# Kernel optimization log

Measured on AMD Instinct MI355X. Metric: run time of the kernel, lower is better.

The kernel has to match this reference:

```python
import jax, jax.numpy as jnp
import numpy as np

HID = 256
N_LAYERS = 4
DT = 0.05
EPS = 1e-3
TMAX = 50


def setup_inputs() -> dict:
    key = jax.random.key(0)
    ks = jax.random.split(key, 7)
    B, S, D = 8, 1024, HID
    s1 = 1.0 / np.sqrt(D)      # fan_in = D for w_state / w_input
    s2 = 1.0 / np.sqrt(2 * D)  # fan_in = 2D for tau_gate linear
    x = jax.random.normal(ks[0], (B, S, D), dtype=jnp.float32)
    Ws = jax.random.uniform(ks[1], (N_LAYERS, D, D), jnp.float32, -s1, s1)
    bs = jax.random.uniform(ks[2], (N_LAYERS, D), jnp.float32, -s1, s1)
    Wi = jax.random.uniform(ks[3], (N_LAYERS, D, D), jnp.float32, -s1, s1)
    bi = jax.random.uniform(ks[4], (N_LAYERS, D), jnp.float32, -s1, s1)
    Wt = jax.random.uniform(ks[5], (N_LAYERS, D, 2 * D), jnp.float32, -s2, s2)
    bt = jax.random.uniform(ks[6], (N_LAYERS, D), jnp.float32, -s2, s2)
    return {"x": x, "Ws": Ws, "bs": bs, "Wi": Wi, "bi": bi, "Wt": Wt, "bt": bt}


def _run(x, Ws, bs, Wi, bi, Wt, bt):
    B, S, D = x.shape

    def layer_fn(cur_in, layer):
        h_prev, Ws_i, bs_i, Wi_i, bi_i, Wt_i, bt_i = layer
        combined = jnp.concatenate([cur_in, h_prev], axis=-1)          # [B,S,2D]
        tau = jax.nn.sigmoid(jnp.einsum('bsk,dk->bsd', combined, Wt_i) + bt_i)
        forcing = jnp.tanh(
            jnp.einsum('bsd,ed->bse', h_prev, Ws_i) + bs_i
            + jnp.einsum('bsd,ed->bse', cur_in, Wi_i) + bi_i
        )
        h_new = jnp.clip(h_prev + DT * (-h_prev / (tau + 1e-6) + forcing), -10.0, 10.0)
        delta = jnp.max(jnp.abs(h_new - h_prev))
        return h_new, (h_new, delta)

    @jax.checkpoint
    def step(carry, i):
        states, result, done = carry
        _, (new_states, deltas) = jax.lax.scan(
            layer_fn, x, (states, Ws, bs, Wi, bi, Wt, bt))
        converged = jnp.max(deltas) < EPS
        states = jnp.where(done, states, new_states)
        # torch returns loop index t at the first converging iteration, else TMAX
        result = jnp.where(done | ~converged, result, i)
        done = done | converged
        return (states, result, done), None

    init = (jnp.zeros((N_LAYERS, B, S, D), x.dtype),
            jnp.array(TMAX, jnp.int32),
            jnp.array(False))
    (states, result, _), _ = jax.lax.scan(step, init, jnp.arange(TMAX, dtype=jnp.int32))
    return states[-1], result


def reference(x, Ws, bs, Wi, bi, Wt, bt):
    return _run(x, Ws, bs, Wi, bi, Wt, bt)
```

## Files before the change

kernel.cpp:

```cpp
#include <hip/hip_runtime.h>
#include <math.h>

#define HID 256
#define TWOH 512
#define ROWS 8192
#define NLAYER 4
#define TMAX 50
#define DT 0.05f
#define EPSC 1e-3f

typedef float f32x4 __attribute__((ext_vector_type(4)));
typedef unsigned char u8;

__device__ inline u8 f32_to_fp8(float v) {
    return (u8)(__builtin_amdgcn_cvt_pk_fp8_f32(v, v, 0, 0) & 0xff);
}
__device__ inline float fp8_to_f32(u8 b) {
    return __builtin_amdgcn_cvt_f32_fp8((int)b, 0);
}

__global__ void pack_w_kernel(const float* __restrict__ Ws,
                              const float* __restrict__ Wi,
                              const float* __restrict__ Wt,
                              u8* __restrict__ Wf) {
    int e = blockIdx.x * 256 + threadIdx.x;
    int j    = e & 7;
    int lane = (e >> 3) & 63;
    int nt   = (e >> 9) & 3;
    int ci   = (e >> 11) & 15;
    int wv   = (e >> 15) & 7;
    int L    = (e >> 18);
    int l15  = lane & 15;
    int quad = lane >> 4;
    int d = wv * 32 + (nt & 1) * 16 + l15;
    int k = ci * 32 + quad * 8 + j;
    float v;
    if ((nt >> 1) == 0) {
        v = Wt[(size_t)L * HID * TWOH + (size_t)d * TWOH + k];
    } else {
        v = (k < HID) ? Wi[(size_t)L * HID * HID + (size_t)d * HID + k]
                      : Ws[(size_t)L * HID * HID + (size_t)d * HID + (k - HID)];
    }
    Wf[e] = f32_to_fp8(v);
}

__global__ void pack_b_kernel(const float* __restrict__ bs,
                              const float* __restrict__ bi,
                              const float* __restrict__ bt,
                              float* __restrict__ bp) {
    int idx = blockIdx.x * 256 + threadIdx.x;
    int L = idx / TWOH;
    int n = idx % TWOH;
    int d = n >> 1;
    bp[idx] = ((n & 1) == 0) ? bt[L * HID + d]
                             : (bs[L * HID + d] + bi[L * HID + d]);
}

__global__ __launch_bounds__(512, 1) void persistent_kernel(
    const float* __restrict__ x,
    const u8* __restrict__ Wf,
    const float* __restrict__ bp,
    float* __restrict__ deltas,
    float* __restrict__ out)
{
    __shared__ u8 sX[32 * 256];
    __shared__ u8 sH[NLAYER][32 * 256];
    __shared__ float2 sBias[NLAYER][256];
    __shared__ float sRed[8];

    const int tid  = threadIdx.x;
    const int lane = tid & 63;
    const int wv   = tid >> 6;
    const int l15  = lane & 15;
    const int quad = lane >> 4;
    const int w32  = wv * 32;
    const size_t rowbase = (size_t)blockIdx.x * 32;

    #pragma unroll
    for (int it = 0; it < 2; ++it) {
        int s = tid + it * 512;
        int r = s >> 5, seg = s & 31;
        const float* gx = x + (rowbase + r) * HID + seg * 8;
        float4 v0 = *(const float4*)gx;
        float4 v1 = *(const float4*)(gx + 4);
        int lo = __builtin_amdgcn_cvt_pk_fp8_f32(v0.x, v0.y, 0, 0);
        lo     = __builtin_amdgcn_cvt_pk_fp8_f32(v0.z, v0.w, lo, 1);
        int hi = __builtin_amdgcn_cvt_pk_fp8_f32(v1.x, v1.y, 0, 0);
        hi     = __builtin_amdgcn_cvt_pk_fp8_f32(v1.z, v1.w, hi, 1);
        long pk = ((long)(unsigned int)lo) | ((long)hi << 32);
        *(long*)&sX[r * 256 + (seg ^ r) * 8] = pk;
    }
    {
        long* hflat = (long*)&sH[0][0];
        #pragma unroll
        for (int it = 0; it < 8; ++it) hflat[tid + it * 512] = 0;
    }
    #pragma unroll
    for (int it = 0; it < 2; ++it) {
        int i = tid + it * 512;
        sBias[i >> 8][i & 255] = *(const float2*)(bp + (i >> 8) * TWOH + 2 * (i & 255));
    }

    __syncthreads();

    for (int t = 0; t < TMAX; ++t) {
        float dmax = 0.0f;
        for (int L = 0; L < NLAYER; ++L) {
            const u8* Alo = (L == 0) ? sX : sH[L - 1];
            u8*       Ahi = sH[L];
            const u8* wb = Wf + ((size_t)(L * 8 + wv) * 32768) + (size_t)lane * 8;

            f32x4 acc[2][4];
            #pragma unroll
            for (int mt = 0; mt < 2; ++mt)
                #pragma unroll
                for (int nt = 0; nt < 4; ++nt)
                    acc[mt][nt] = (f32x4){0.f, 0.f, 0.f, 0.f};

            long bb[4][4];
            #pragma unroll
            for (int pi = 0; pi < 4; ++pi)
                #pragma unroll
                for (int nt = 0; nt < 4; ++nt)
                    bb[pi][nt] = *(const long*)(wb + (size_t)(pi * 4 + nt) * 512);

            #pragma unroll
            for (int ci = 0; ci < 16; ++ci) {
                const int p = ci & 3;
                const u8* Asrc = (ci < 8) ? Alo : Ahi;
                const int seg = (ci & 7) * 4 + quad;
                long a[2];
                #pragma unroll
                for (int mt = 0; mt < 2; ++mt) {
                    int row = mt * 16 + l15;
                    a[mt] = *(const long*)&Asrc[row * 256 + (seg ^ row) * 8];
                }
                #pragma unroll
                for (int mt = 0; mt < 2; ++mt)
                    #pragma unroll
                    for (int nt = 0; nt < 4; ++nt)
                        acc[mt][nt] = __builtin_amdgcn_mfma_f32_16x16x32_fp8_fp8(
                            a[mt], bb[p][nt], acc[mt][nt], 0, 0, 0);
                if (ci + 4 < 16) {
                    #pragma unroll
                    for (int nt = 0; nt < 4; ++nt)
                        bb[p][nt] = *(const long*)(wb + (size_t)((ci + 4) * 4 + nt) * 512);
                }
            }

            __syncthreads();

            #pragma unroll
            for (int ntp = 0; ntp < 2; ++ntp) {
                const int d = w32 + ntp * 16 + l15;
                const float2 bb2 = sBias[L][d];
                const int seg = d >> 3, dlow = d & 7;
                #pragma unroll
                for (int mt = 0; mt < 2; ++mt) {
                    #pragma unroll
                    for (int r = 0; r < 4; ++r) {
                        float tpre = acc[mt][ntp][r]     + bb2.x;
                        float fpre = acc[mt][ntp + 2][r] + bb2.y;
                        tpre = fminf(30.f, fmaxf(-30.f, tpre));
                        fpre = fminf(15.f, fmaxf(-15.f, fpre));
                        float u   = __expf(-tpre);
                        float den = 1.0f + 1e-6f + 1e-6f * u;
                        float rcp = __builtin_amdgcn_rcpf(den);
                        float e2  = __expf(2.0f * fpre);
                        float r2  = __builtin_amdgcn_rcpf(e2 + 1.0f);
                        float fo  = (e2 - 1.0f) * r2;
                        const int row = mt * 16 + quad * 4 + r;
                        const int idx = row * 256 + (seg ^ row) * 8 + dlow;
                        float h  = fp8_to_f32(Ahi[idx]);
                        float g  = h * (1.0f + u) * rcp;
                        float nv = h + DT * (fo - g);
                        nv = fminf(10.0f, fmaxf(-10.0f, nv));
                        Ahi[idx] = f32_to_fp8(nv);
                        dmax = fmaxf(dmax, fabsf(nv - h));
                    }
                }
            }
            if (L == NLAYER - 1) {
                #pragma unroll
                for (int off = 32; off > 0; off >>= 1)
                    dmax = fmaxf(dmax, __shfl_xor(dmax, off));
                if (lane == 0) sRed[wv] = dmax;
            }
            __syncthreads();
        }

        if (tid == 0) {
            float m = sRed[0];
            #pragma unroll
            for (int w = 1; w < 8; ++w) m = fmaxf(m, sRed[w]);
            atomicMax((unsigned int*)(deltas + t), __float_as_uint(m));
        }
    }

    #pragma unroll
    for (int it = 0; it < 2; ++it) {
        int s = tid + it * 512;
        int r = s >> 5, seg = s & 31;
        long v = *(const long*)&sH[NLAYER - 1][r * 256 + (seg ^ r) * 8];
        int lo = (int)(v & 0xffffffffl);
        int hi = (int)(v >> 32);
        float* go = out + (rowbase + r) * HID + seg * 8;
        float4 o0, o1;
        o0.x = __builtin_amdgcn_cvt_f32_fp8(lo, 0);
        o0.y = __builtin_amdgcn_cvt_f32_fp8(lo, 1);
        o0.z = __builtin_amdgcn_cvt_f32_fp8(lo, 2);
        o0.w = __builtin_amdgcn_cvt_f32_fp8(lo, 3);
        o1.x = __builtin_amdgcn_cvt_f32_fp8(hi, 0);
        o1.y = __builtin_amdgcn_cvt_f32_fp8(hi, 1);
        o1.z = __builtin_amdgcn_cvt_f32_fp8(hi, 2);
        o1.w = __builtin_amdgcn_cvt_f32_fp8(hi, 3);
        *(float4*)go = o0;
        *(float4*)(go + 4) = o1;
    }
}

__global__ void result_kernel(const float* __restrict__ deltas,
                              float* __restrict__ out) {
    if (threadIdx.x == 0) {
        int res = TMAX;
        for (int t = 0; t < TMAX; ++t) {
            if (deltas[t] < EPSC) { res = t; break; }
        }
        out[(size_t)ROWS * HID] = (float)res;
    }
}

extern "C" void kernel_launch(void* const* d_in, const int* in_sizes, int n_in,
                              void* d_out, int out_size, void* d_ws, size_t ws_size,
                              hipStream_t stream) {
    const float* x  = (const float*)d_in[0];
    const float* Ws = (const float*)d_in[1];
    const float* bs = (const float*)d_in[2];
    const float* Wi = (const float*)d_in[3];
    const float* bi = (const float*)d_in[4];
    const float* Wt = (const float*)d_in[5];
    const float* bt = (const float*)d_in[6];
    float* out = (float*)d_out;

    char* p = (char*)d_ws;
    u8*    Wf     = (u8*)p;    p += (size_t)NLAYER * TWOH * TWOH;
    float* bp     = (float*)p; p += (size_t)NLAYER * TWOH * sizeof(float);
    float* deltas = (float*)p; p += 64 * sizeof(float);

    hipMemsetAsync(deltas, 0, 64 * sizeof(float), stream);
    pack_w_kernel<<<(NLAYER * TWOH * TWOH) / 256, 256, 0, stream>>>(Ws, Wi, Wt, Wf);
    pack_b_kernel<<<(NLAYER * TWOH) / 256, 256, 0, stream>>>(bs, bi, bt, bp);

    persistent_kernel<<<256, 512, 0, stream>>>(x, Wf, bp, deltas, out);
    result_kernel<<<1, 64, 0, stream>>>(deltas, out);
}
```

Measured before the change: 1.228 ms.

## Double-buffer hidden states to cut per-layer barriers and widen weight loads

Hidden states are now ping-pong buffered across timesteps. Each layer reads the previous timestep's own-layer state first and syncs only once, midway, before reading the lower layer's new state. This removes one of the two block barriers per layer. The weight packing is reordered so each lane loads 16-byte vectors instead of 8-byte ones. The per-wave delta max now goes straight to a global atomic instead of through a shared reduction, which adds more atomics per block and doubles the hidden-state shared memory.

```diff
diff --git a/kernel.cpp b/kernel.cpp
--- a/kernel.cpp
+++ b/kernel.cpp
@@ -10,6 +10,7 @@
 #define EPSC 1e-3f
 
 typedef float f32x4 __attribute__((ext_vector_type(4)));
+typedef long  long2v __attribute__((ext_vector_type(2)));
 typedef unsigned char u8;
 
 __device__ inline u8 f32_to_fp8(float v) {
@@ -25,17 +26,18 @@
                               u8* __restrict__ Wf) {
     int e = blockIdx.x * 256 + threadIdx.x;
     int j    = e & 7;
-    int lane = (e >> 3) & 63;
-    int nt   = (e >> 9) & 3;
+    int h    = (e >> 3) & 1;
+    int lane = (e >> 4) & 63;
+    int g    = (e >> 10) & 1;
     int ci   = (e >> 11) & 15;
     int wv   = (e >> 15) & 7;
     int L    = (e >> 18);
     int l15  = lane & 15;
     int quad = lane >> 4;
-    int d = wv * 32 + (nt & 1) * 16 + l15;
+    int d = wv * 32 + h * 16 + l15;
     int k = ci * 32 + quad * 8 + j;
     float v;
-    if ((nt >> 1) == 0) {
+    if (g == 0) {
         v = Wt[(size_t)L * HID * TWOH + (size_t)d * TWOH + k];
     } else {
         v = (k < HID) ? Wi[(size_t)L * HID * HID + (size_t)d * HID + k]
@@ -64,9 +66,8 @@
     float* __restrict__ out)
 {
     __shared__ u8 sX[32 * 256];
-    __shared__ u8 sH[NLAYER][32 * 256];
+    __shared__ u8 sH[2][NLAYER][32 * 256];
     __shared__ float2 sBias[NLAYER][256];
-    __shared__ float sRed[8];
 
     const int tid  = threadIdx.x;
     const int lane = tid & 63;
@@ -91,9 +92,9 @@
         *(long*)&sX[r * 256 + (seg ^ r) * 8] = pk;
     }
     {
-        long* hflat = (long*)&sH[0][0];
+        long* hflat = (long*)&sH[0][0][0];
         #pragma unroll
-        for (int it = 0; it < 8; ++it) hflat[tid + it * 512] = 0;
+        for (int it = 0; it < 16; ++it) hflat[tid + it * 512] = 0;
     }
     #pragma unroll
     for (int it = 0; it < 2; ++it) {
@@ -103,64 +104,69 @@
 
     __syncthreads();
 
+    #pragma unroll 1
     for (int t = 0; t < TMAX; ++t) {
+        const int rs = t & 1, ws = rs ^ 1;
         float dmax = 0.0f;
+        #pragma unroll
         for (int L = 0; L < NLAYER; ++L) {
-            const u8* Alo = (L == 0) ? sX : sH[L - 1];
-            u8*       Ahi = sH[L];
-            const u8* wb = Wf + ((size_t)(L * 8 + wv) * 32768) + (size_t)lane * 8;
+            const u8* Ahi = &sH[rs][L][0];
+            const u8* Alo = (L == 0) ? sX : &sH[ws][L - 1][0];
+            u8*       Hout = &sH[ws][L][0];
+            const u8* wb = Wf + ((size_t)(L * 8 + wv) << 15) + (size_t)lane * 16;
 
             f32x4 acc[2][4];
             #pragma unroll
             for (int mt = 0; mt < 2; ++mt)
                 #pragma unroll
-                for (int nt = 0; nt < 4; ++nt)
-                    acc[mt][nt] = (f32x4){0.f, 0.f, 0.f, 0.f};
-
-            long bb[4][4];
-            #pragma unroll
-            for (int pi = 0; pi < 4; ++pi)
-                #pragma unroll
-                for (int nt = 0; nt < 4; ++nt)
-                    bb[pi][nt] = *(const long*)(wb + (size_t)(pi * 4 + nt) * 512);
-
-            #pragma unroll
-            for (int ci = 0; ci < 16; ++ci) {
-                const int p = ci & 3;
-                const u8* Asrc = (ci < 8) ? Alo : Ahi;
+                for (int n = 0; n < 4; ++n)
+                    acc[mt][n] = (f32x4){0.f, 0.f, 0.f, 0.f};
+
+            long2v bb[2][2];
+            #pragma unroll
+            for (int pi = 0; pi < 2; ++pi)
+                #pragma unroll
+                for (int g = 0; g < 2; ++g)
+                    bb[pi][g] = *(const long2v*)(wb + (size_t)(((8 + pi) * 2 + g) << 10));
+
+            #pragma unroll
+            for (int s = 0; s < 16; ++s) {
+                const int ci = (s < 8) ? (s + 8) : (s - 8);
+                const int p = s & 1;
+                if (s == 8) __syncthreads();
+                const u8* Asrc = (s < 8) ? Ahi : Alo;
                 const int seg = (ci & 7) * 4 + quad;
                 long a[2];
                 #pragma unroll
                 for (int mt = 0; mt < 2; ++mt) {
-                    int row = mt * 16 + l15;
+                    const int row = mt * 16 + l15;
                     a[mt] = *(const long*)&Asrc[row * 256 + (seg ^ row) * 8];
                 }
                 #pragma unroll
                 for (int mt = 0; mt < 2; ++mt)
                     #pragma unroll
-                    for (int nt = 0; nt < 4; ++nt)
-                        acc[mt][nt] = __builtin_amdgcn_mfma_f32_16x16x32_fp8_fp8(
-                            a[mt], bb[p][nt], acc[mt][nt], 0, 0, 0);
-                if (ci + 4 < 16) {
+                    for (int n = 0; n < 4; ++n)
+                        acc[mt][n] = __builtin_amdgcn_mfma_f32_16x16x32_fp8_fp8(
+                            a[mt], bb[p][n >> 1][n & 1], acc[mt][n], 0, 0, 0);
+                if (s + 2 < 16) {
+                    const int nci = (s + 2 < 8) ? (s + 10) : (s - 6);
                     #pragma unroll
-                    for (int nt = 0; nt < 4; ++nt)
-                        bb[p][nt] = *(const long*)(wb + (size_t)((ci + 4) * 4 + nt) * 512);
+                    for (int g = 0; g < 2; ++g)
+                        bb[p][g] = *(const long2v*)(wb + (size_t)((nci * 2 + g) << 10));
                 }
             }
 
-            __syncthreads();
-
             #pragma unroll
             for (int ntp = 0; ntp < 2; ++ntp) {
                 const int d = w32 + ntp * 16 + l15;
-                const float2 bb2 = sBias[L][d];
+                const float2 b2 = sBias[L][d];
                 const int seg = d >> 3, dlow = d & 7;
                 #pragma unroll
                 for (int mt = 0; mt < 2; ++mt) {
                     #pragma unroll
                     for (int r = 0; r < 4; ++r) {
-                        float tpre = acc[mt][ntp][r]     + bb2.x;
-                        float fpre = acc[mt][ntp + 2][r] + bb2.y;
+                        float tpre = acc[mt][ntp][r]     + b2.x;
+                        float fpre = acc[mt][ntp + 2][r] + b2.y;
                         tpre = fminf(30.f, fmaxf(-30.f, tpre));
                         fpre = fminf(15.f, fmaxf(-15.f, fpre));
                         float u   = __expf(-tpre);
@@ -172,10 +178,10 @@
                         const int row = mt * 16 + quad * 4 + r;
                         const int idx = row * 256 + (seg ^ row) * 8 + dlow;
                         float h  = fp8_to_f32(Ahi[idx]);
-                        float g  = h * (1.0f + u) * rcp;
-                        float nv = h + DT * (fo - g);
+                        float gq = h * (1.0f + u) * rcp;
+                        float nv = h + DT * (fo - gq);
                         nv = fminf(10.0f, fmaxf(-10.0f, nv));
-                        Ahi[idx] = f32_to_fp8(nv);
+                        Hout[idx] = f32_to_fp8(nv);
                         dmax = fmaxf(dmax, fabsf(nv - h));
                     }
                 }
@@ -184,38 +190,36 @@
                 #pragma unroll
                 for (int off = 32; off > 0; off >>= 1)
                     dmax = fmaxf(dmax, __shfl_xor(dmax, off));
-                if (lane == 0) sRed[wv] = dmax;
+                if (lane == 0)
+                    atomicMax((unsigned int*)(deltas + t), __float_as_uint(dmax));
             }
-            __syncthreads();
         }
-
-        if (tid == 0) {
-            float m = sRed[0];
-            #pragma unroll
-            for (int w = 1; w < 8; ++w) m = fmaxf(m, sRed[w]);
-            atomicMax((unsigned int*)(deltas + t), __float_as_uint(m));
+    }
+
+    __syncthreads();
+
+    {
+        const u8* fin = &sH[((TMAX - 1) & 1) ^ 1][NLAYER - 1][0];
+        #pragma unroll
+        for (int it = 0; it < 2; ++it) {
+            int s = tid + it * 512;
+            int r = s >> 5, seg = s & 31;
+            long v = *(const long*)&fin[r * 256 + (seg ^ r) * 8];
+            int lo = (int)(v & 0xffffffffl);
+            int hi = (int)(v >> 32);
+            float* go = out + (rowbase + r) * HID + seg * 8;
+            float4 o0, o1;
+            o0.x = __builtin_amdgcn_cvt_f32_fp8(lo, 0);
+            o0.y = __builtin_amdgcn_cvt_f32_fp8(lo, 1);
+            o0.z = __builtin_amdgcn_cvt_f32_fp8(lo, 2);
+            o0.w = __builtin_amdgcn_cvt_f32_fp8(lo, 3);
+            o1.x = __builtin_amdgcn_cvt_f32_fp8(hi, 0);
+            o1.y = __builtin_amdgcn_cvt_f32_fp8(hi, 1);
+            o1.z = __builtin_amdgcn_cvt_f32_fp8(hi, 2);
+            o1.w = __builtin_amdgcn_cvt_f32_fp8(hi, 3);
+            *(float4*)go = o0;
+            *(float4*)(go + 4) = o1;
         }
-    }
-
-    #pragma unroll
-    for (int it = 0; it < 2; ++it) {
-        int s = tid + it * 512;
-        int r = s >> 5, seg = s & 31;
-        long v = *(const long*)&sH[NLAYER - 1][r * 256 + (seg ^ r) * 8];
-        int lo = (int)(v & 0xffffffffl);
-        int hi = (int)(v >> 32);
-        float* go = out + (rowbase + r) * HID + seg * 8;
-        float4 o0, o1;
-        o0.x = __builtin_amdgcn_cvt_f32_fp8(lo, 0);
-        o0.y = __builtin_amdgcn_cvt_f32_fp8(lo, 1);
-        o0.z = __builtin_amdgcn_cvt_f32_fp8(lo, 2);
-        o0.w = __builtin_amdgcn_cvt_f32_fp8(lo, 3);
-        o1.x = __builtin_amdgcn_cvt_f32_fp8(hi, 0);
-        o1.y = __builtin_amdgcn_cvt_f32_fp8(hi, 1);
-        o1.z = __builtin_amdgcn_cvt_f32_fp8(hi, 2);
-        o1.w = __builtin_amdgcn_cvt_f32_fp8(hi, 3);
-        *(float4*)go = o0;
-        *(float4*)(go + 4) = o1;
     }
 }
 
```

Measured after the change: 2.377 ms. 93.6% more time.
